# Optimization experiments

Measured on AMD Instinct MI355X. Metric: run time of the kernel, lower is better.

## Reference

```python
import jax, jax.numpy as jnp
import numpy as np

WIN = 9
EPS = 1e-06

def _box_conv(x, win):
    C = x.shape[1]
    k = jnp.ones((C, C, win, win), dtype=x.dtype)
    pad = win // 2
    return jax.lax.conv_general_dilated(
        x, k, window_strides=(1, 1), padding=[(pad, pad), (pad, pad)],
        dimension_numbers=('NCHW', 'OIHW', 'NCHW'))

def setup_inputs() -> dict:
    key = jax.random.key(0)
    k1, k2 = jax.random.split(key)
    shape = (32, 1, 512, 512)
    template = jax.random.uniform(k1, shape, dtype=jnp.float32)
    image = jax.random.uniform(k2, shape, dtype=jnp.float32)
    return {"template": template, "image": image}

def reference(template, image):
    I2 = template * template
    J2 = image * image
    IJ = image * template

    I_sum = _box_conv(template, WIN)
    J_sum = _box_conv(image, WIN)
    I2_sum = _box_conv(I2, WIN)
    J2_sum = _box_conv(J2, WIN)
    IJ_sum = _box_conv(IJ, WIN)

    win_area = float(WIN * WIN)
    u_I = I_sum / win_area
    u_J = J_sum / win_area

    cross = IJ_sum - u_J * I_sum - u_I * J_sum + u_I * u_J * win_area
    I_var = I2_sum - 2.0 * u_I * I_sum + u_I * u_I * win_area
    J_var = J2_sum - 2.0 * u_J * J_sum + u_J * u_J * win_area

    scores = cross / (jnp.sqrt(I_var) * jnp.sqrt(J_var) + EPS)
    return 1.0 - jnp.mean(scores)
```

## Files before the change

### kernel.cpp

```cpp
#include <hip/hip_runtime.h>
#include <math.h>

#define IMG    512
#define IMG2   (IMG*IMG)
#define TC     64
#define TR     32
#define ECC    72
#define PITCH  33
#define NBATCH 32
#define NBLOCKS ((IMG/TC)*(IMG/TR)*NBATCH)
#define NPIX   8388608.0f

typedef float f2 __attribute__((ext_vector_type(2)));
typedef float f4 __attribute__((ext_vector_type(4)));

__device__ __forceinline__ float pk_bf16(float a, float b) {
    float r;
    asm("v_cvt_pk_bf16_f32 %0, %1, %2" : "=v"(r) : "v"(a), "v"(b));
    return r;
}

__global__ __launch_bounds__(256, 4)
void lncc_main(const float* __restrict__ Tm, const float* __restrict__ Im,
               float* __restrict__ partial)
{
    __shared__ f4 V[ECC * PITCH];
    __shared__ float wsum[4];

    const int tid = threadIdx.x;
    const int x0 = blockIdx.x * TC;
    const int y0 = blockIdx.y * TR;
    const size_t base = (size_t)blockIdx.z * IMG2;
    const float* tb = Tm + base;
    const float* ib = Im + base;

    if (tid < 2 * ECC) {
        const int ec    = tid % ECC;
        const int strip = tid / ECC;
        const int r0    = strip * 16;
        const int gx    = x0 + ec - 4;
        const float xm  = ((unsigned)gx < IMG) ? 1.0f : 0.0f;
        const int gxc   = gx < 0 ? 0 : (gx > IMG - 1 ? IMG - 1 : gx);
        const int Y     = y0 + r0 - 4;

        f2 ring[9];
        f2 w01 = {0.f, 0.f}, w23 = {0.f, 0.f};
        float w4 = 0.f;

        #pragma unroll
        for (int j = 0; j < 24; ++j) {
            const int gy  = Y + j;
            const float m = ((unsigned)gy < IMG) ? xm : 0.0f;
            const int gyc = gy < 0 ? 0 : (gy > IMG - 1 ? IMG - 1 : gy);
            const int off = (gyc << 9) + gxc;
            f2 tv;
            tv.x = tb[off] * m;
            tv.y = ib[off] * m;
            w01 += tv;
            w23 += tv * tv;
            w4  = fmaf(tv.x, tv.y, w4);
            ring[j % 9] = tv;
            if (j >= 8) {
                const int k = j - 8;
                f4 e;
                e.x = w01.x; e.y = w01.y;
                e.z = pk_bf16(w23.x, w23.y);
                e.w = pk_bf16(w4, w4);
                V[ec * PITCH + r0 + k] = e;
                const f2 o = ring[k % 9];
                w01 -= o;
                w23 -= o * o;
                w4  = fmaf(-o.x, o.y, w4);
            }
        }
    }
    __syncthreads();

    float lsum = 0.f;
    {
        const int row = tid & 31;
        const int cb  = (tid >> 5) * 8;
        f2 r01[9], r23[9];
        float r4[9];
        f2 W01 = {0.f, 0.f}, W23 = {0.f, 0.f};
        float W4 = 0.f;
        const float inv81 = 1.0f / 81.0f;

        #pragma unroll
        for (int k = 0; k < 16; ++k) {
            const f4 e = V[(cb + k) * PITCH + row];
            const unsigned u23 = __float_as_uint(e.z);
            const unsigned u4  = __float_as_uint(e.w);
            f2 h01; h01.x = e.x; h01.y = e.y;
            f2 h23;
            h23.x = __uint_as_float(u23 << 16);
            h23.y = __uint_as_float(u23 & 0xffff0000u);
            const float h4 = __uint_as_float(u4 & 0xffff0000u);
            W01 += h01; W23 += h23; W4 += h4;
            const int ri = k % 9;
            r01[ri] = h01; r23[ri] = h23; r4[ri] = h4;
            if (k >= 8) {
                const float t0 = W01.x * inv81;
                const float t1 = W01.y * inv81;
                const float cross = fmaf(-t0, W01.y, W4);
                const float Iv    = fmaf(-t0, W01.x, W23.x);
                const float Jv    = fmaf(-t1, W01.y, W23.y);
                const float den   = fmaf(Iv, Jv, 1e-12f);
                lsum += cross * __builtin_amdgcn_rsqf(den);
                const int o = (k - 8) % 9;
                W01 -= r01[o]; W23 -= r23[o]; W4 -= r4[o];
            }
        }
    }

    #pragma unroll
    for (int d = 32; d >= 1; d >>= 1) lsum += __shfl_down(lsum, d, 64);
    if ((tid & 63) == 0) wsum[tid >> 6] = lsum;
    __syncthreads();
    if (tid == 0) {
        const int bid = (blockIdx.z * gridDim.y + blockIdx.y) * gridDim.x + blockIdx.x;
        partial[bid] = wsum[0] + wsum[1] + wsum[2] + wsum[3];
    }
}

__global__ __launch_bounds__(256)
void lncc_reduce(const float* __restrict__ partial, float* __restrict__ out)
{
    __shared__ float ws[4];
    const int tid = threadIdx.x;
    float s = 0.f;
    #pragma unroll
    for (int i = 0; i < NBLOCKS / 256; ++i) s += partial[tid + i * 256];
    #pragma unroll
    for (int d = 32; d >= 1; d >>= 1) s += __shfl_down(s, d, 64);
    if ((tid & 63) == 0) ws[tid >> 6] = s;
    __syncthreads();
    if (tid == 0) out[0] = 1.0f - (ws[0] + ws[1] + ws[2] + ws[3]) / NPIX;
}

extern "C" void kernel_launch(void* const* d_in, const int* in_sizes, int n_in,
                              void* d_out, int out_size, void* d_ws, size_t ws_size,
                              hipStream_t stream)
{
    (void)in_sizes; (void)n_in; (void)out_size; (void)ws_size;
    const float* Tm = (const float*)d_in[0];
    const float* Im = (const float*)d_in[1];
    float* out  = (float*)d_out;
    float* part = (float*)d_ws;

    dim3 grid(IMG / TC, IMG / TR, NBATCH);
    lncc_main<<<grid, 256, 0, stream>>>(Tm, Im, part);
    lncc_reduce<<<1, 256, 0, stream>>>(part, out);
}
```

Measured before the change: 28.62 us.

## Add interior-tile fast path with float2 loads and swizzle LDS rows

Tiles that do not touch the image border now take a separate path. It drops clamping and masking, loads two adjacent columns per thread with float2 loads, and writes two LDS entries, so 72 threads do the vertical pass instead of 144. LDS row indices are XOR-swizzled in both the write and read phases to reduce bank conflicts. The trade-off is fewer active threads in the vertical pass, with more work and registers per thread.

```diff
diff --git a/kernel.cpp b/kernel.cpp
--- a/kernel.cpp
+++ b/kernel.cpp
@@ -7,6 +7,7 @@
 #define TR     32
 #define ECC    72
 #define PITCH  33
+#define LDSN   (ECC*PITCH)
 #define NBATCH 32
 #define NBLOCKS ((IMG/TC)*(IMG/TR)*NBATCH)
 #define NPIX   8388608.0f
@@ -20,11 +21,13 @@
     return r;
 }
 
+__device__ __forceinline__ int swz(int row) { return row ^ ((row >> 3) & 3); }
+
 __global__ __launch_bounds__(256, 4)
 void lncc_main(const float* __restrict__ Tm, const float* __restrict__ Im,
                float* __restrict__ partial)
 {
-    __shared__ f4 V[ECC * PITCH];
+    __shared__ f4 V[LDSN];
     __shared__ float wsum[4];
 
     const int tid = threadIdx.x;
@@ -34,43 +37,86 @@
     const float* tb = Tm + base;
     const float* ib = Im + base;
 
-    if (tid < 2 * ECC) {
-        const int ec    = tid % ECC;
-        const int strip = tid / ECC;
-        const int r0    = strip * 16;
-        const int gx    = x0 + ec - 4;
-        const float xm  = ((unsigned)gx < IMG) ? 1.0f : 0.0f;
-        const int gxc   = gx < 0 ? 0 : (gx > IMG - 1 ? IMG - 1 : gx);
-        const int Y     = y0 + r0 - 4;
-
-        f2 ring[9];
-        f2 w01 = {0.f, 0.f}, w23 = {0.f, 0.f};
-        float w4 = 0.f;
-
-        #pragma unroll
-        for (int j = 0; j < 24; ++j) {
-            const int gy  = Y + j;
-            const float m = ((unsigned)gy < IMG) ? xm : 0.0f;
-            const int gyc = gy < 0 ? 0 : (gy > IMG - 1 ? IMG - 1 : gy);
-            const int off = (gyc << 9) + gxc;
-            f2 tv;
-            tv.x = tb[off] * m;
-            tv.y = ib[off] * m;
-            w01 += tv;
-            w23 += tv * tv;
-            w4  = fmaf(tv.x, tv.y, w4);
-            ring[j % 9] = tv;
-            if (j >= 8) {
-                const int k = j - 8;
-                f4 e;
-                e.x = w01.x; e.y = w01.y;
-                e.z = pk_bf16(w23.x, w23.y);
-                e.w = pk_bf16(w4, w4);
-                V[ec * PITCH + r0 + k] = e;
-                const f2 o = ring[k % 9];
-                w01 -= o;
-                w23 -= o * o;
-                w4  = fmaf(-o.x, o.y, w4);
+    const bool interior = (blockIdx.x >= 1) & (blockIdx.x <= 6) &
+                          (blockIdx.y >= 1) & (blockIdx.y <= 14);
+
+    if (interior) {
+        if (tid < 72) {
+            const int pr    = tid % 36;
+            const int strip = tid / 36;
+            const int r0    = strip * 16;
+            const int c2    = pr * 2;
+            const int off0  = (y0 + r0 - 4) * IMG + (x0 + c2 - 4);
+            const float* tp = tb + off0;
+            const float* ip = ib + off0;
+
+            f2 rt[9], rv[9];
+            f2 s0 = {0.f,0.f}, s1 = {0.f,0.f}, s2 = {0.f,0.f},
+               s3 = {0.f,0.f}, s4 = {0.f,0.f};
+
+            #pragma unroll
+            for (int j = 0; j < 24; ++j) {
+                const f2 t = *(const f2*)(tp + j * IMG);
+                const f2 v = *(const f2*)(ip + j * IMG);
+                s0 += t; s1 += v;
+                s2 += t * t; s3 += v * v; s4 += t * v;
+                rt[j % 9] = t; rv[j % 9] = v;
+                if (j >= 8) {
+                    const int k   = j - 8;
+                    const int row = r0 + k;
+                    f4 e0, e1;
+                    e0.x = s0.x; e0.y = s1.x;
+                    e0.z = pk_bf16(s2.x, s3.x); e0.w = pk_bf16(s4.x, s4.x);
+                    e1.x = s0.y; e1.y = s1.y;
+                    e1.z = pk_bf16(s2.y, s3.y); e1.w = pk_bf16(s4.y, s4.y);
+                    const int rw = swz(row);
+                    V[c2 * PITCH + rw]       = e0;
+                    V[(c2 + 1) * PITCH + rw] = e1;
+                    const f2 ot = rt[k % 9], ov = rv[k % 9];
+                    s0 -= ot; s1 -= ov;
+                    s2 -= ot * ot; s3 -= ov * ov; s4 -= ot * ov;
+                }
+            }
+        }
+    } else {
+        if (tid < 144) {
+            const int ec    = tid % ECC;
+            const int strip = tid / ECC;
+            const int r0    = strip * 16;
+            const int gx    = x0 + ec - 4;
+            const float xm  = ((unsigned)gx < IMG) ? 1.0f : 0.0f;
+            const int gxc   = gx < 0 ? 0 : (gx > IMG - 1 ? IMG - 1 : gx);
+            const int Y     = y0 + r0 - 4;
+
+            f2 ring[9];
+            f2 w01 = {0.f,0.f}, w23 = {0.f,0.f};
+            float w4 = 0.f;
+
+            #pragma unroll
+            for (int j = 0; j < 24; ++j) {
+                const int gy  = Y + j;
+                const float m = ((unsigned)gy < IMG) ? xm : 0.0f;
+                const int gyc = gy < 0 ? 0 : (gy > IMG - 1 ? IMG - 1 : gy);
+                const int off = (gyc << 9) + gxc;
+                f2 tv;
+                tv.x = tb[off] * m;
+                tv.y = ib[off] * m;
+                w01 += tv;
+                w23 += tv * tv;
+                w4  = fmaf(tv.x, tv.y, w4);
+                ring[j % 9] = tv;
+                if (j >= 8) {
+                    const int k = j - 8;
+                    f4 e;
+                    e.x = w01.x; e.y = w01.y;
+                    e.z = pk_bf16(w23.x, w23.y);
+                    e.w = pk_bf16(w4, w4);
+                    V[ec * PITCH + swz(r0 + k)] = e;
+                    const f2 o = ring[k % 9];
+                    w01 -= o;
+                    w23 -= o * o;
+                    w4  = fmaf(-o.x, o.y, w4);
+                }
             }
         }
     }
@@ -78,17 +124,19 @@
 
     float lsum = 0.f;
     {
-        const int row = tid & 31;
-        const int cb  = (tid >> 5) * 8;
+        const int row  = tid & 31;
+        const int cb   = (tid >> 5) * 8;
+        const f4* src  = &V[cb * PITCH + swz(row)];
+
         f2 r01[9], r23[9];
         float r4[9];
-        f2 W01 = {0.f, 0.f}, W23 = {0.f, 0.f};
+        f2 W01 = {0.f,0.f}, W23 = {0.f,0.f};
         float W4 = 0.f;
         const float inv81 = 1.0f / 81.0f;
 
         #pragma unroll
         for (int k = 0; k < 16; ++k) {
-            const f4 e = V[(cb + k) * PITCH + row];
+            const f4 e = src[k * PITCH];
             const unsigned u23 = __float_as_uint(e.z);
             const unsigned u4  = __float_as_uint(e.w);
             f2 h01; h01.x = e.x; h01.y = e.y;
```

Measured after the change: 31.65 us. +10.6%, slower.

## Compact LDS to 12-byte bf16 entries, add interior fast path, three strips

Applied to the files above, without the earlier changes.

Packs all five vertical window sums as bf16, stored as a uint2 plus a u32 per entry, to cut LDS footprint and traffic. Phase 1 now uses three row strips of 11 per column so more threads load. Interior blocks skip the clamp and mask arithmetic. Occupancy hint rises to 5 blocks per CU. Storing the first-order sums in bf16 adds rounding error that the variance cancellation may amplify.

```diff
diff --git a/kernel.cpp b/kernel.cpp
--- a/kernel.cpp
+++ b/kernel.cpp
@@ -11,20 +11,20 @@
 #define NBLOCKS ((IMG/TC)*(IMG/TR)*NBATCH)
 #define NPIX   8388608.0f
 
-typedef float f2 __attribute__((ext_vector_type(2)));
-typedef float f4 __attribute__((ext_vector_type(4)));
+typedef unsigned int u32;
 
-__device__ __forceinline__ float pk_bf16(float a, float b) {
+__device__ __forceinline__ u32 pk_bf16(float a, float b) {
     float r;
     asm("v_cvt_pk_bf16_f32 %0, %1, %2" : "=v"(r) : "v"(a), "v"(b));
-    return r;
+    return __float_as_uint(r);
 }
 
-__global__ __launch_bounds__(256, 4)
+__global__ __launch_bounds__(256, 5)
 void lncc_main(const float* __restrict__ Tm, const float* __restrict__ Im,
                float* __restrict__ partial)
 {
-    __shared__ f4 V[ECC * PITCH];
+    __shared__ uint2 AB[ECC * PITCH];
+    __shared__ u32   Cc[ECC * PITCH];
     __shared__ float wsum[4];
 
     const int tid = threadIdx.x;
@@ -34,43 +34,60 @@
     const float* tb = Tm + base;
     const float* ib = Im + base;
 
-    if (tid < 2 * ECC) {
+    const bool interior = (blockIdx.x - 1u < 6u) & (blockIdx.y - 1u < 14u);
+
+    if (tid < 3 * ECC) {
         const int ec    = tid % ECC;
         const int strip = tid / ECC;
-        const int r0    = strip * 16;
-        const int gx    = x0 + ec - 4;
-        const float xm  = ((unsigned)gx < IMG) ? 1.0f : 0.0f;
-        const int gxc   = gx < 0 ? 0 : (gx > IMG - 1 ? IMG - 1 : gx);
-        const int Y     = y0 + r0 - 4;
+        const int r0    = strip * 11;
 
-        f2 ring[9];
-        f2 w01 = {0.f, 0.f}, w23 = {0.f, 0.f};
-        float w4 = 0.f;
+        float rt[9], rv[9];
+        float s0 = 0.f, s1 = 0.f, s2 = 0.f, s3 = 0.f, s4 = 0.f;
 
-        #pragma unroll
-        for (int j = 0; j < 24; ++j) {
-            const int gy  = Y + j;
-            const float m = ((unsigned)gy < IMG) ? xm : 0.0f;
-            const int gyc = gy < 0 ? 0 : (gy > IMG - 1 ? IMG - 1 : gy);
-            const int off = (gyc << 9) + gxc;
-            f2 tv;
-            tv.x = tb[off] * m;
-            tv.y = ib[off] * m;
-            w01 += tv;
-            w23 += tv * tv;
-            w4  = fmaf(tv.x, tv.y, w4);
-            ring[j % 9] = tv;
-            if (j >= 8) {
-                const int k = j - 8;
-                f4 e;
-                e.x = w01.x; e.y = w01.y;
-                e.z = pk_bf16(w23.x, w23.y);
-                e.w = pk_bf16(w4, w4);
-                V[ec * PITCH + r0 + k] = e;
-                const f2 o = ring[k % 9];
-                w01 -= o;
-                w23 -= o * o;
-                w4  = fmaf(-o.x, o.y, w4);
+        if (interior) {
+            const int off0 = (y0 + r0 - 4) * IMG + (x0 + ec - 4);
+            const float* tp = tb + off0;
+            const float* ip = ib + off0;
+            #pragma unroll
+            for (int j = 0; j < 19; ++j) {
+                const float t = tp[j * IMG];
+                const float v = ip[j * IMG];
+                s0 += t; s1 += v;
+                s2 = fmaf(t, t, s2); s3 = fmaf(v, v, s3); s4 = fmaf(t, v, s4);
+                rt[j % 9] = t; rv[j % 9] = v;
+                if (j >= 8) {
+                    const int idx = ec * PITCH + r0 + (j - 8);
+                    AB[idx] = make_uint2(pk_bf16(s0, s1), pk_bf16(s2, s3));
+                    Cc[idx] = pk_bf16(s4, s4);
+                    const float ot = rt[(j - 8) % 9], ov = rv[(j - 8) % 9];
+                    s0 -= ot; s1 -= ov;
+                    s2 = fmaf(-ot, ot, s2); s3 = fmaf(-ov, ov, s3); s4 = fmaf(-ot, ov, s4);
+                }
+            }
+        } else {
+            const int gx   = x0 + ec - 4;
+            const float xm = ((unsigned)gx < IMG) ? 1.0f : 0.0f;
+            const int gxc  = gx < 0 ? 0 : (gx > IMG - 1 ? IMG - 1 : gx);
+            const int Y    = y0 + r0 - 4;
+            #pragma unroll
+            for (int j = 0; j < 19; ++j) {
+                const int gy  = Y + j;
+                const float m = ((unsigned)gy < IMG) ? xm : 0.0f;
+                const int gyc = gy < 0 ? 0 : (gy > IMG - 1 ? IMG - 1 : gy);
+                const int off = (gyc << 9) + gxc;
+                const float t = tb[off] * m;
+                const float v = ib[off] * m;
+                s0 += t; s1 += v;
+                s2 = fmaf(t, t, s2); s3 = fmaf(v, v, s3); s4 = fmaf(t, v, s4);
+                rt[j % 9] = t; rv[j % 9] = v;
+                if (j >= 8) {
+                    const int idx = ec * PITCH + r0 + (j - 8);
+                    AB[idx] = make_uint2(pk_bf16(s0, s1), pk_bf16(s2, s3));
+                    Cc[idx] = pk_bf16(s4, s4);
+                    const float ot = rt[(j - 8) % 9], ov = rv[(j - 8) % 9];
+                    s0 -= ot; s1 -= ov;
+                    s2 = fmaf(-ot, ot, s2); s3 = fmaf(-ov, ov, s3); s4 = fmaf(-ot, ov, s4);
+                }
             }
         }
     }
@@ -79,36 +96,37 @@
     float lsum = 0.f;
     {
         const int row = tid & 31;
-        const int cb  = (tid >> 5) * 8;
-        f2 r01[9], r23[9];
-        float r4[9];
-        f2 W01 = {0.f, 0.f}, W23 = {0.f, 0.f};
-        float W4 = 0.f;
+        const int b0  = (tid >> 5) * 8 * PITCH + row;
+        float W0 = 0.f, W1 = 0.f, W2 = 0.f, W3 = 0.f, W4 = 0.f;
+        uint2 rab[9];
+        u32   rc[9];
         const float inv81 = 1.0f / 81.0f;
 
         #pragma unroll
         for (int k = 0; k < 16; ++k) {
-            const f4 e = V[(cb + k) * PITCH + row];
-            const unsigned u23 = __float_as_uint(e.z);
-            const unsigned u4  = __float_as_uint(e.w);
-            f2 h01; h01.x = e.x; h01.y = e.y;
-            f2 h23;
-            h23.x = __uint_as_float(u23 << 16);
-            h23.y = __uint_as_float(u23 & 0xffff0000u);
-            const float h4 = __uint_as_float(u4 & 0xffff0000u);
-            W01 += h01; W23 += h23; W4 += h4;
-            const int ri = k % 9;
-            r01[ri] = h01; r23[ri] = h23; r4[ri] = h4;
+            const uint2 ab = AB[b0 + k * PITCH];
+            const u32   c  = Cc[b0 + k * PITCH];
+            W0 += __uint_as_float(ab.x << 16);
+            W1 += __uint_as_float(ab.x & 0xffff0000u);
+            W2 += __uint_as_float(ab.y << 16);
+            W3 += __uint_as_float(ab.y & 0xffff0000u);
+            W4 += __uint_as_float(c & 0xffff0000u);
+            rab[k % 9] = ab; rc[k % 9] = c;
             if (k >= 8) {
-                const float t0 = W01.x * inv81;
-                const float t1 = W01.y * inv81;
-                const float cross = fmaf(-t0, W01.y, W4);
-                const float Iv    = fmaf(-t0, W01.x, W23.x);
-                const float Jv    = fmaf(-t1, W01.y, W23.y);
+                const float t0 = W0 * inv81;
+                const float t1 = W1 * inv81;
+                const float cross = fmaf(-t0, W1, W4);
+                const float Iv    = fmaf(-t0, W0, W2);
+                const float Jv    = fmaf(-t1, W1, W3);
                 const float den   = fmaf(Iv, Jv, 1e-12f);
                 lsum += cross * __builtin_amdgcn_rsqf(den);
-                const int o = (k - 8) % 9;
-                W01 -= r01[o]; W23 -= r23[o]; W4 -= r4[o];
+                const uint2 oab = rab[(k - 8) % 9];
+                const u32   oc  = rc[(k - 8) % 9];
+                W0 -= __uint_as_float(oab.x << 16);
+                W1 -= __uint_as_float(oab.x & 0xffff0000u);
+                W2 -= __uint_as_float(oab.y << 16);
+                W3 -= __uint_as_float(oab.y & 0xffff0000u);
+                W4 -= __uint_as_float(oc & 0xffff0000u);
             }
         }
     }
```

Measured after the change: 27.68 us. 3.3% less time.
